# Optimization experiments

Measured on AMD Instinct MI355X. Metric: run time of the kernel, lower is better.

## Reference

```python
import jax, jax.numpy as jnp
import numpy as np

B, C, T_IN = 32, 512, 1024
T_OUT = 4096  # fixed total expanded length (all rows of durations sum to this)


def setup_inputs() -> dict:
    key = jax.random.key(0)
    k_enc, k_cut = jax.random.split(key)
    encodings = jax.random.normal(k_enc, (B, C, T_IN), dtype=jnp.float32)
    # durations: nonnegative ints summing exactly to T_OUT per row, mean ~4.
    # Build as diffs of sorted random cut points in [0, T_OUT].
    cuts = jnp.sort(jax.random.randint(k_cut, (B, T_IN - 1), 0, T_OUT), axis=1)
    lo = jnp.zeros((B, 1), dtype=cuts.dtype)
    hi = jnp.full((B, 1), T_OUT, dtype=cuts.dtype)
    bounds = jnp.concatenate([lo, cuts, hi], axis=1)  # [B, T_IN+1]
    durations = (bounds[:, 1:] - bounds[:, :-1]).astype(jnp.int64)  # [B, T_IN]
    return {"encodings": encodings, "durations": durations}


def reference(encodings, durations):
    # Fused length regulation: instead of per-batch repeat_interleave + stack,
    # compute the gather index map from cumulative durations in one pass.
    # out[b, :, t] = encodings[b, :, j] where j = searchsorted(cumsum(dur[b]), t, 'right')
    cum = jnp.cumsum(durations, axis=1)  # [B, T_IN], last col == T_OUT
    t = jnp.arange(T_OUT)  # [T_OUT]
    idx = jax.vmap(lambda c: jnp.searchsorted(c, t, side="right"))(cum)  # [B, T_OUT]
    # gather along time axis, broadcast over channels
    return jnp.take_along_axis(encodings, idx[:, None, :], axis=2)  # [B, C, T_OUT]
```

## Files before the change

kernel.cpp:

```cpp
#include <hip/hip_runtime.h>
#include <hip/hip_bf16.h>

#define B_DIM 32
#define C_DIM 512
#define T_IN 1024
#define T_OUT 4096
#define CPB 4

typedef float nfloat4 __attribute__((ext_vector_type(4)));
typedef int nint4 __attribute__((ext_vector_type(4)));

__global__ __launch_bounds__(256) void build_idx_kernel(
    const int* __restrict__ dur, int* __restrict__ idx) {
    __shared__ int s_cum[T_IN];
    __shared__ int s_part[256];

    const int b = blockIdx.x;
    const int tid = threadIdx.x;

    nint4 v = ((const nint4*)(dur + b * T_IN))[tid];
    int c1 = v.x, c2 = c1 + v.y, c3 = c2 + v.z, c4 = c3 + v.w;

    s_part[tid] = c4;
    __syncthreads();
    #pragma unroll
    for (int off = 1; off < 256; off <<= 1) {
        int val = s_part[tid];
        int add = (tid >= off) ? s_part[tid - off] : 0;
        __syncthreads();
        s_part[tid] = val + add;
        __syncthreads();
    }
    int prefix = s_part[tid] - c4;

    nint4 cumv;
    cumv.x = prefix + c1;
    cumv.y = prefix + c2;
    cumv.z = prefix + c3;
    cumv.w = prefix + c4;
    ((nint4*)s_cum)[tid] = cumv;
    __syncthreads();

    int* row = idx + b * T_OUT;
    #pragma unroll
    for (int k = 0; k < 16; ++k) {
        const int t = k * 256 + tid;
        int lo = 0, hi = T_IN - 1;
        #pragma unroll
        for (int s = 0; s < 10; ++s) {
            int mid = (lo + hi) >> 1;
            bool gt = s_cum[mid] > t;
            hi = gt ? mid : hi;
            lo = gt ? lo : mid + 1;
        }
        row[t] = lo;
    }
}

__global__ __launch_bounds__(256) void gather_kernel(
    const float* __restrict__ enc, const int* __restrict__ idx,
    float* __restrict__ out) {
    __shared__ float s_rows[CPB][T_IN];

    const int blk = blockIdx.x;
    const int b = blk >> 7;
    const int c0 = (blk & 127) * CPB;
    const int tid = threadIdx.x;

    const float* enc_base = enc + ((size_t)(b * C_DIM + c0)) * T_IN;
    #pragma unroll
    for (int cc = 0; cc < CPB; ++cc) {
        nfloat4 v = __builtin_nontemporal_load(
            ((const nfloat4*)(enc_base + cc * T_IN)) + tid);
        ((nfloat4*)s_rows[cc])[tid] = v;
    }
    __syncthreads();

    const nint4* idx_row = (const nint4*)(idx + b * T_OUT);
    float* out_base = out + ((size_t)(b * C_DIM + c0)) * T_OUT;

    #pragma unroll
    for (int g = 0; g < 4; ++g) {
        const int t4 = g * 256 + tid;
        nint4 j = idx_row[t4];
        #pragma unroll
        for (int cc = 0; cc < CPB; ++cc) {
            nfloat4 o;
            o.x = s_rows[cc][j.x];
            o.y = s_rows[cc][j.y];
            o.z = s_rows[cc][j.z];
            o.w = s_rows[cc][j.w];
            __builtin_nontemporal_store(
                o, ((nfloat4*)(out_base + (size_t)cc * T_OUT)) + t4);
        }
    }
}

extern "C" void kernel_launch(void* const* d_in, const int* in_sizes, int n_in,
                              void* d_out, int out_size, void* d_ws, size_t ws_size,
                              hipStream_t stream) {
    const float* enc = (const float*)d_in[0];
    const int* dur = (const int*)d_in[1];
    float* out = (float*)d_out;
    int* idx = (int*)d_ws;

    build_idx_kernel<<<B_DIM, 256, 0, stream>>>(dur, idx);
    gather_kernel<<<B_DIM * (C_DIM / CPB), 256, 0, stream>>>(enc, idx, out);
}
```

Baseline: 312.8 us.

## Split index build across blocks and pipeline gather loads with direct-to-LDS copies

The index-building kernel now runs PARTS blocks per batch row, each recomputing the prefix sum and searching only its slice of output positions. This removes the serialized 32-block launch. The gather kernel loads encoder rows straight into LDS with global_load_lds, in two halves. It prefetches the index vectors into registers and writes outputs for the first two channels while the last two are still loading, using a manual vmcnt wait and barrier. The hand-counted waitcnt depends on the exact instruction order the compiler emits, which makes it fragile.

```diff
diff --git a/kernel.cpp b/kernel.cpp
--- a/kernel.cpp
+++ b/kernel.cpp
@@ -1,21 +1,27 @@
 #include <hip/hip_runtime.h>
-#include <hip/hip_bf16.h>
 
 #define B_DIM 32
 #define C_DIM 512
 #define T_IN 1024
 #define T_OUT 4096
 #define CPB 4
+#define PARTS 8
 
 typedef float nfloat4 __attribute__((ext_vector_type(4)));
 typedef int nint4 __attribute__((ext_vector_type(4)));
 
+#define GLDS(lptr, gptr)                                                      \
+    __builtin_amdgcn_global_load_lds(                                         \
+        (const __attribute__((address_space(1))) unsigned int*)(gptr),        \
+        (__attribute__((address_space(3))) unsigned int*)(lptr), 16, 0, 0)
+
 __global__ __launch_bounds__(256) void build_idx_kernel(
     const int* __restrict__ dur, int* __restrict__ idx) {
-    __shared__ int s_cum[T_IN];
+    __shared__ __align__(16) int s_cum[T_IN];
     __shared__ int s_part[256];
 
     const int b = blockIdx.x;
+    const int part = blockIdx.y;
     const int tid = threadIdx.x;
 
     nint4 v = ((const nint4*)(dur + b * T_IN))[tid];
@@ -41,10 +47,10 @@
     ((nint4*)s_cum)[tid] = cumv;
     __syncthreads();
 
-    int* row = idx + b * T_OUT;
+    int* row = idx + b * T_OUT + part * (T_OUT / PARTS);
     #pragma unroll
-    for (int k = 0; k < 16; ++k) {
-        const int t = k * 256 + tid;
+    for (int k = 0; k < T_OUT / PARTS / 256; ++k) {
+        const int t = part * (T_OUT / PARTS) + k * 256 + tid;
         int lo = 0, hi = T_IN - 1;
         #pragma unroll
         for (int s = 0; s < 10; ++s) {
@@ -53,45 +59,69 @@
             hi = gt ? mid : hi;
             lo = gt ? lo : mid + 1;
         }
-        row[t] = lo;
+        row[k * 256 + tid] = lo;
     }
 }
 
 __global__ __launch_bounds__(256) void gather_kernel(
     const float* __restrict__ enc, const int* __restrict__ idx,
     float* __restrict__ out) {
-    __shared__ float s_rows[CPB][T_IN];
+    __shared__ __align__(16) float s_rows[CPB][T_IN];
 
     const int blk = blockIdx.x;
     const int b = blk >> 7;
     const int c0 = (blk & 127) * CPB;
     const int tid = threadIdx.x;
+    const int wbase = (tid >> 6) << 8;
 
     const float* enc_base = enc + ((size_t)(b * C_DIM + c0)) * T_IN;
+
+    GLDS(&s_rows[0][wbase], enc_base + 0 * T_IN + tid * 4);
+    GLDS(&s_rows[1][wbase], enc_base + 1 * T_IN + tid * 4);
+
+    const nint4* idx_row = (const nint4*)(idx + b * T_OUT);
+    nint4 jj[4];
     #pragma unroll
-    for (int cc = 0; cc < CPB; ++cc) {
-        nfloat4 v = __builtin_nontemporal_load(
-            ((const nfloat4*)(enc_base + cc * T_IN)) + tid);
-        ((nfloat4*)s_rows[cc])[tid] = v;
-    }
+    for (int g = 0; g < 4; ++g) jj[g] = idx_row[g * 256 + tid];
+
     __syncthreads();
 
-    const nint4* idx_row = (const nint4*)(idx + b * T_OUT);
+    GLDS(&s_rows[2][wbase], enc_base + 2 * T_IN + tid * 4);
+    GLDS(&s_rows[3][wbase], enc_base + 3 * T_IN + tid * 4);
+    asm volatile("" ::: "memory");
+
     float* out_base = out + ((size_t)(b * C_DIM + c0)) * T_OUT;
 
     #pragma unroll
-    for (int g = 0; g < 4; ++g) {
-        const int t4 = g * 256 + tid;
-        nint4 j = idx_row[t4];
+    for (int cc = 0; cc < 2; ++cc) {
         #pragma unroll
-        for (int cc = 0; cc < CPB; ++cc) {
+        for (int g = 0; g < 4; ++g) {
+            nint4 j = jj[g];
             nfloat4 o;
             o.x = s_rows[cc][j.x];
             o.y = s_rows[cc][j.y];
             o.z = s_rows[cc][j.z];
             o.w = s_rows[cc][j.w];
             __builtin_nontemporal_store(
-                o, ((nfloat4*)(out_base + (size_t)cc * T_OUT)) + t4);
+                o, ((nfloat4*)(out_base + (size_t)cc * T_OUT)) + g * 256 + tid);
+        }
+    }
+
+    asm volatile("s_waitcnt vmcnt(8)" ::: "memory");
+    __builtin_amdgcn_s_barrier();
+
+    #pragma unroll
+    for (int cc = 2; cc < CPB; ++cc) {
+        #pragma unroll
+        for (int g = 0; g < 4; ++g) {
+            nint4 j = jj[g];
+            nfloat4 o;
+            o.x = s_rows[cc][j.x];
+            o.y = s_rows[cc][j.y];
+            o.z = s_rows[cc][j.z];
+            o.w = s_rows[cc][j.w];
+            __builtin_nontemporal_store(
+                o, ((nfloat4*)(out_base + (size_t)cc * T_OUT)) + g * 256 + tid);
         }
     }
 }
@@ -104,6 +134,6 @@
     float* out = (float*)d_out;
     int* idx = (int*)d_ws;
 
-    build_idx_kernel<<<B_DIM, 256, 0, stream>>>(dur, idx);
+    build_idx_kernel<<<dim3(B_DIM, PARTS), 256, 0, stream>>>(dur, idx);
     gather_kernel<<<B_DIM * (C_DIM / CPB), 256, 0, stream>>>(enc, idx, out);
 }
```

Result: no change. 316.8 us (+1.3%).
